# Performance work log

Measured on AMD Instinct MI355X. Metric: run time of the kernel, lower is better.

Reference implementation:

```python
import jax, jax.numpy as jnp
import numpy as np

HEAD_DIM = 64
CLIP = 64  # clipping_distance
B, S = 32, 1024


def setup_inputs() -> dict:
    key = jax.random.key(0)
    kq, kk, kv, km, kt = jax.random.split(key, 5)
    q = jax.random.normal(kq, (B, S, HEAD_DIM), dtype=jnp.float32)
    k = jax.random.normal(kk, (B, S, HEAD_DIM), dtype=jnp.float32)
    v = jax.random.normal(kv, (B, S, HEAD_DIM), dtype=jnp.float32)
    mask = jax.random.randint(km, (B, S, S), 0, 2).astype(jnp.bool_)
    pos_table = jax.random.normal(kt, (2 * CLIP + 1, HEAD_DIM), dtype=jnp.float32)
    return {"q": q, "k": k, "v": v, "mask": mask, "pos_table": pos_table}


def reference(q, k, v, mask, pos_table):
    scaling = 1.0 / np.sqrt(HEAD_DIM).astype(np.float32)
    Sq, Sk = q.shape[1], k.shape[1]
    # relative positions k_idx - q_idx, clipped to [-CLIP, CLIP]
    rel = jnp.arange(Sk)[None, :] - jnp.arange(Sq)[:, None]      # [Sq, Sk]
    idx = jnp.clip(rel, -CLIP, CLIP) + CLIP                      # [Sq, Sk]
    pe = pos_table[idx]                                          # [Sq, Sk, D]
    # content logits + relative positional logits
    logits = jnp.einsum('bqd,bkd->bqk', q, k) + jnp.einsum('bqd,qkd->bqk', q, pe)
    logits = logits * scaling
    logits = jnp.where(mask, -jnp.inf, logits)
    attn = jax.nn.softmax(logits, axis=-1)                       # [B, Sq, Sk]
    return jnp.einsum('bqk,bkd->bqd', attn, v)
```

## Files before the change

kernel.cpp:

```cpp
#include <hip/hip_runtime.h>
#include <stdint.h>

#define BATCH 32
#define SEQ   1024
#define DIM   64
#define NKT   (SEQ / 64)

typedef uint8_t  u8;
typedef uint16_t u16;
typedef uint32_t u32;
typedef unsigned long long u64;
typedef __attribute__((ext_vector_type(8))) __bf16 bf16x8;
typedef __attribute__((ext_vector_type(4))) float  f32x4;
typedef __attribute__((ext_vector_type(4))) u32    u32x4;

__device__ __forceinline__ float fexp2(float x) {
#if __has_builtin(__builtin_amdgcn_exp2f)
    return __builtin_amdgcn_exp2f(x);
#else
    return exp2f(x);
#endif
}

__device__ __forceinline__ u16 f2bf(float f) {
    u32 x = __builtin_bit_cast(u32, f);
    x += 0x7FFFu + ((x >> 16) & 1u);
    return (u16)(x >> 16);
}

__device__ __forceinline__ bf16x8 cvt8(const float* __restrict__ p) {
    f32x4 a = *reinterpret_cast<const f32x4*>(p);
    f32x4 b = *reinterpret_cast<const f32x4*>(p + 4);
    u16 t[8];
    t[0] = f2bf(a[0]); t[1] = f2bf(a[1]); t[2] = f2bf(a[2]); t[3] = f2bf(a[3]);
    t[4] = f2bf(b[0]); t[5] = f2bf(b[1]); t[6] = f2bf(b[2]); t[7] = f2bf(b[3]);
    return __builtin_bit_cast(bf16x8, *reinterpret_cast<u32x4*>(t));
}

__device__ __forceinline__ bf16x8 cvt8s(const float* __restrict__ p, float s) {
    f32x4 a = *reinterpret_cast<const f32x4*>(p);
    f32x4 b = *reinterpret_cast<const f32x4*>(p + 4);
    u16 t[8];
    t[0] = f2bf(a[0] * s); t[1] = f2bf(a[1] * s); t[2] = f2bf(a[2] * s); t[3] = f2bf(a[3] * s);
    t[4] = f2bf(b[0] * s); t[5] = f2bf(b[1] * s); t[6] = f2bf(b[2] * s); t[7] = f2bf(b[3] * s);
    return __builtin_bit_cast(bf16x8, *reinterpret_cast<u32x4*>(t));
}

__device__ __forceinline__ bf16x8 ldg8(const u16* p) {
    u32x4 u = *reinterpret_cast<const u32x4*>(p);
    return __builtin_bit_cast(bf16x8, u);
}

__device__ __forceinline__ u32 pack4(u32x4 a) {
    return (u32)(a[0] != 0) | ((u32)(a[1] != 0) << 8) |
           ((u32)(a[2] != 0) << 16) | ((u32)(a[3] != 0) << 24);
}

__global__ __launch_bounds__(256) void prep_kv(
    const float* __restrict__ kg, const float* __restrict__ vg,
    u16* __restrict__ kb, u16* __restrict__ vtb_) {
    __shared__ u16 tile[64][72];
    const int t  = threadIdx.x;
    const int b  = blockIdx.x >> 4;
    const int k0 = (blockIdx.x & 15) * 64;

    {
        int kk = t >> 2;
        int d0 = (t & 3) * 16;
        const float* src = kg + ((size_t)b * SEQ + k0 + kk) * DIM + d0;
        u16 tmp[16];
#pragma unroll
        for (int i = 0; i < 4; ++i) {
            f32x4 a = *reinterpret_cast<const f32x4*>(src + i * 4);
            tmp[i * 4 + 0] = f2bf(a[0]); tmp[i * 4 + 1] = f2bf(a[1]);
            tmp[i * 4 + 2] = f2bf(a[2]); tmp[i * 4 + 3] = f2bf(a[3]);
        }
        u16* dst = kb + ((size_t)b * SEQ + k0 + kk) * DIM + d0;
        *reinterpret_cast<u32x4*>(dst)     = *reinterpret_cast<u32x4*>(tmp);
        *reinterpret_cast<u32x4*>(dst + 8) = *reinterpret_cast<u32x4*>(tmp + 8);
    }
    {
        const float* vb = vg + (size_t)b * SEQ * DIM;
        int kk = t >> 2;
        int d0 = (t & 3) * 16;
        const float* src = vb + (size_t)(k0 + kk) * DIM + d0;
        u16 tmp[16];
#pragma unroll
        for (int i = 0; i < 4; ++i) {
            f32x4 a = *reinterpret_cast<const f32x4*>(src + i * 4);
            tmp[i * 4 + 0] = f2bf(a[0]); tmp[i * 4 + 1] = f2bf(a[1]);
            tmp[i * 4 + 2] = f2bf(a[2]); tmp[i * 4 + 3] = f2bf(a[3]);
        }
        *reinterpret_cast<u32x4*>(&tile[kk][d0])     = *reinterpret_cast<u32x4*>(tmp);
        *reinterpret_cast<u32x4*>(&tile[kk][d0 + 8]) = *reinterpret_cast<u32x4*>(tmp + 8);
    }
    __syncthreads();
    u16* vtb = vtb_ + (size_t)b * DIM * SEQ;
#pragma unroll
    for (int i = 0; i < 2; ++i) {
        int d  = t / 8 + i * 32;
        int ks = (t % 8) * 8;
        u16 tmp[8];
#pragma unroll
        for (int j = 0; j < 8; ++j) tmp[j] = tile[ks + j][d];
        *reinterpret_cast<u32x4*>(vtb + (size_t)d * SEQ + k0 + ks) =
            *reinterpret_cast<u32x4*>(tmp);
    }
}

__global__ __launch_bounds__(512, 4) void attn_fast8(
    const float* __restrict__ qg, const u16* __restrict__ kbf,
    const u16* __restrict__ vt, const int* __restrict__ maskg,
    const float* __restrict__ ptg, float* __restrict__ outg) {
    __shared__ float qp[64][132];
    __shared__ u16   plds[8][16][72];
    __shared__ u8    mlds[8][16][64];

    const int b    = blockIdx.y;
    const int q0   = blockIdx.x * 64;
    const int tid  = threadIdx.x;
    const int wave = tid >> 6;
    const int lane = tid & 63;
    const int wq   = wave & 3;
    const int wk   = wave >> 2;
    const int quad = lane >> 4;
    const int c16  = lane & 15;

    const float SC = 0.125f * 1.44269504088896340736f;

    const float* qb = qg + ((size_t)b * SEQ + q0) * DIM;

    const bf16x8 qA0 = cvt8s(qb + (size_t)(wq * 16 + c16) * DIM + quad * 8, SC);
    const bf16x8 qA1 = cvt8s(qb + (size_t)(wq * 16 + c16) * DIM + 32 + quad * 8, SC);

    {
        const int jt0 = wk ? 5 : 0, jt1 = wk ? 9 : 5;
        for (int jt = jt0; jt < jt1; ++jt) {
            int j0 = jt * 16;
            int jr = min(j0 + c16, 128);
            bf16x8 b0 = cvt8(ptg + (size_t)jr * DIM + quad * 8);
            bf16x8 b1 = cvt8(ptg + (size_t)jr * DIM + 32 + quad * 8);
            f32x4 acc = {0.f, 0.f, 0.f, 0.f};
            acc = __builtin_amdgcn_mfma_f32_16x16x32_bf16(qA0, b0, acc, 0, 0, 0);
            acc = __builtin_amdgcn_mfma_f32_16x16x32_bf16(qA1, b1, acc, 0, 0, 0);
            int jcol = j0 + c16;
            if (jcol <= 128) {
#pragma unroll
                for (int r = 0; r < 4; ++r)
                    qp[wq * 16 + quad * 4 + r][jcol] = acc[r];
            }
        }
    }
    __syncthreads();

    const u16* kb_base  = kbf + (size_t)b * SEQ * DIM;
    const u16* vtb_base = vt  + (size_t)b * DIM * SEQ;

    const int* mrow = maskg + ((size_t)b * SEQ + q0 + wq * 16 + (lane >> 2)) * SEQ +
                      (lane & 3) * 16;

    u32x4 ma, mbv, mc, md;
    {
        const int* p = mrow + (size_t)(wk * 8) * 64;
        ma  = *reinterpret_cast<const u32x4*>(p);
        mbv = *reinterpret_cast<const u32x4*>(p + 4);
        mc  = *reinterpret_cast<const u32x4*>(p + 8);
        md  = *reinterpret_cast<const u32x4*>(p + 12);
    }

    float l_part[4];
    f32x4 O[4];
#pragma unroll
    for (int r = 0; r < 4; ++r) l_part[r] = 0.f;
#pragma unroll
    for (int d = 0; d < 4; ++d) O[d] = f32x4{0.f, 0.f, 0.f, 0.f};

#pragma unroll
    for (int gg = 0; gg < 2; ++gg) {
#pragma unroll 1
        for (int t = 0; t < 4; ++t) {
            const int kt = wk * 8 + gg * 4 + t;
            const int k0 = kt * 64;

            {
                u32x4 pk;
                pk[0] = pack4(ma); pk[1] = pack4(mbv);
                pk[2] = pack4(mc); pk[3] = pack4(md);
                *reinterpret_cast<u32x4*>(&mlds[wave][lane >> 2][(lane & 3) * 16]) = pk;
            }
            {
                const int* p = mrow + (size_t)((kt + 1) & 15) * 64;
                ma  = *reinterpret_cast<const u32x4*>(p);
                mbv = *reinterpret_cast<const u32x4*>(p + 4);
                mc  = *reinterpret_cast<const u32x4*>(p + 8);
                md  = *reinterpret_cast<const u32x4*>(p + 12);
            }

            f32x4 S[4];
            __builtin_amdgcn_s_setprio(1);
#pragma unroll
            for (int sub = 0; sub < 4; ++sub) {
                const u16* kr = kb_base + (size_t)(k0 + sub * 16 + c16) * DIM;
                bf16x8 kf0 = ldg8(kr + quad * 8);
                bf16x8 kf1 = ldg8(kr + 32 + quad * 8);
                f32x4 acc = {0.f, 0.f, 0.f, 0.f};
                acc = __builtin_amdgcn_mfma_f32_16x16x32_bf16(qA0, kf0, acc, 0, 0, 0);
                acc = __builtin_amdgcn_mfma_f32_16x16x32_bf16(qA1, kf1, acc, 0, 0, 0);
                S[sub] = acc;
            }
            __builtin_amdgcn_s_setprio(0);

#pragma unroll
            for (int r = 0; r < 4; ++r) {
                const int row_l = quad * 4 + r;
                const int row_g = q0 + wq * 16 + row_l;
                float rs = 0.f;
#pragma unroll
                for (int sub = 0; sub < 4; ++sub) {
                    int col_g = k0 + sub * 16 + c16;
                    int rel = col_g - row_g;
                    rel = rel < -64 ? -64 : (rel > 64 ? 64 : rel);
                    float x = S[sub][r] + qp[wq * 16 + row_l][rel + 64];
                    u8 mv = mlds[wave][row_l][sub * 16 + c16];
                    float e = mv ? 0.f : fexp2(x);
                    rs += e;
                    plds[wave][row_l][sub * 16 + c16] = f2bf(e);
                }
                l_part[r] += rs;
            }

            bf16x8 pA0 = *reinterpret_cast<bf16x8*>(&plds[wave][c16][quad * 8]);
            bf16x8 pA1 = *reinterpret_cast<bf16x8*>(&plds[wave][c16][32 + quad * 8]);
            __builtin_amdgcn_s_setprio(1);
#pragma unroll
            for (int d = 0; d < 4; ++d) {
                const u16* vr = vtb_base + (size_t)(d * 16 + c16) * SEQ + k0;
                bf16x8 vf0 = ldg8(vr + quad * 8);
                bf16x8 vf1 = ldg8(vr + 32 + quad * 8);
                O[d] = __builtin_amdgcn_mfma_f32_16x16x32_bf16(pA0, vf0, O[d], 0, 0, 0);
                O[d] = __builtin_amdgcn_mfma_f32_16x16x32_bf16(pA1, vf1, O[d], 0, 0, 0);
            }
            __builtin_amdgcn_s_setprio(0);
        }
    }

    float l_run[4];
#pragma unroll
    for (int r = 0; r < 4; ++r) {
        float rs = l_part[r];
        rs += __shfl_xor(rs, 1);
        rs += __shfl_xor(rs, 2);
        rs += __shfl_xor(rs, 4);
        rs += __shfl_xor(rs, 8);
        l_run[r] = rs;
    }

    __syncthreads();
    float* cmb = &qp[0][0];
    const int cbase = (wq * 64 + lane) * 24;
    if (wk == 1) {
#pragma unroll
        for (int r = 0; r < 4; ++r) cmb[cbase + r] = l_run[r];
#pragma unroll
        for (int d = 0; d < 4; ++d)
#pragma unroll
            for (int r = 0; r < 4; ++r)
                cmb[cbase + 4 + d * 4 + r] = O[d][r];
    }
    __syncthreads();
    if (wk == 0) {
        float* ob = outg + ((size_t)b * SEQ + q0) * DIM;
#pragma unroll
        for (int r = 0; r < 4; ++r) {
            float inv = 1.f / (l_run[r] + cmb[cbase + r]);
            int row_l = wq * 16 + quad * 4 + r;
#pragma unroll
            for (int d = 0; d < 4; ++d) {
                float o = O[d][r] + cmb[cbase + 4 + d * 4 + r];
                ob[(size_t)row_l * DIM + d * 16 + c16] = o * inv;
            }
        }
    }
}

__global__ __launch_bounds__(256) void vt_kernel(const float* __restrict__ v,
                                                 u16* __restrict__ vt) {
    __shared__ u16 tile[64][72];
    const int b  = blockIdx.y;
    const int k0 = blockIdx.x * 64;
    const int t  = threadIdx.x;
    const float* vb  = v  + (size_t)b * SEQ * DIM;
    u16*         vtb = vt + (size_t)b * DIM * SEQ;

    {
        int kk = t >> 2;
        int d0 = (t & 3) * 16;
        const float* src = vb + (size_t)(k0 + kk) * DIM + d0;
        u16 tmp[16];
#pragma unroll
        for (int i = 0; i < 4; ++i) {
            f32x4 a = *reinterpret_cast<const f32x4*>(src + i * 4);
            tmp[i * 4 + 0] = f2bf(a[0]); tmp[i * 4 + 1] = f2bf(a[1]);
            tmp[i * 4 + 2] = f2bf(a[2]); tmp[i * 4 + 3] = f2bf(a[3]);
        }
        *reinterpret_cast<u32x4*>(&tile[kk][d0])     = *reinterpret_cast<u32x4*>(tmp);
        *reinterpret_cast<u32x4*>(&tile[kk][d0 + 8]) = *reinterpret_cast<u32x4*>(tmp + 8);
    }
    __syncthreads();
#pragma unroll
    for (int i = 0; i < 2; ++i) {
        int d  = t / 8 + i * 32;
        int ks = (t % 8) * 8;
        u16 tmp[8];
#pragma unroll
        for (int j = 0; j < 8; ++j) tmp[j] = tile[ks + j][d];
        *reinterpret_cast<u32x4*>(vtb + (size_t)d * SEQ + k0 + ks) =
            *reinterpret_cast<u32x4*>(tmp);
    }
}

template <bool USE_VT>
__global__ __launch_bounds__(256, 2) void attn_kernel(
    const float* __restrict__ qg, const float* __restrict__ kg,
    const void* __restrict__ vgv, const int* __restrict__ maskg,
    const float* __restrict__ ptg, float* __restrict__ outg) {
    __shared__ float qp[64][132];
    __shared__ int   mlds[4][16][68];
    __shared__ u16   plds[4][16][72];

    const int b    = blockIdx.y;
    const int q0   = blockIdx.x * 64;
    const int tid  = threadIdx.x;
    const int wave = tid >> 6;
    const int lane = tid & 63;
    const int quad = lane >> 4;
    const int c16  = lane & 15;

    const float* qb = qg + ((size_t)b * SEQ + q0) * DIM;
    const float* kb = kg + (size_t)b * SEQ * DIM;
    const int*   mb = maskg + ((size_t)b * SEQ + q0) * SEQ;

    const bf16x8 qA0 = cvt8(qb + (size_t)(wave * 16 + c16) * DIM + quad * 8);
    const bf16x8 qA1 = cvt8(qb + (size_t)(wave * 16 + c16) * DIM + 32 + quad * 8);

    for (int jt = 0; jt < 9; ++jt) {
        int j0 = jt * 16;
        int jr = min(j0 + c16, 128);
        bf16x8 b0 = cvt8(ptg + (size_t)jr * DIM + quad * 8);
        bf16x8 b1 = cvt8(ptg + (size_t)jr * DIM + 32 + quad * 8);
        f32x4 acc = {0.f, 0.f, 0.f, 0.f};
        acc = __builtin_amdgcn_mfma_f32_16x16x32_bf16(qA0, b0, acc, 0, 0, 0);
        acc = __builtin_amdgcn_mfma_f32_16x16x32_bf16(qA1, b1, acc, 0, 0, 0);
        int jcol = j0 + c16;
        if (jcol <= 128) {
#pragma unroll
            for (int r = 0; r < 4; ++r)
                qp[wave * 16 + quad * 4 + r][jcol] = acc[r];
        }
    }

    float m_run[4], l_run[4];
    f32x4 O[4];
#pragma unroll
    for (int r = 0; r < 4; ++r) { m_run[r] = -1e30f; l_run[r] = 0.f; }
#pragma unroll
    for (int d = 0; d < 4; ++d) O[d] = f32x4{0.f, 0.f, 0.f, 0.f};

#pragma unroll 1
    for (int kt = 0; kt < NKT; ++kt) {
        const int k0 = kt * 64;
        {
            int row_l = lane >> 2;
            const int* mrow = mb + (size_t)(wave * 16 + row_l) * SEQ + k0;
#pragma unroll
            for (int i = 0; i < 4; ++i) {
                int seg = (lane & 3) + i * 4;
                *reinterpret_cast<u32x4*>(&mlds[wave][row_l][seg * 4]) =
                    *reinterpret_cast<const u32x4*>(mrow + seg * 4);
            }
        }

        f32x4 S[4];
#pragma unroll
        for (int sub = 0; sub < 4; ++sub) {
            const float* kr = kb + (size_t)(k0 + sub * 16 + c16) * DIM;
            bf16x8 kb0 = cvt8(kr + quad * 8);
            bf16x8 kb1 = cvt8(kr + 32 + quad * 8);
            f32x4 acc = {0.f, 0.f, 0.f, 0.f};
            acc = __builtin_amdgcn_mfma_f32_16x16x32_bf16(qA0, kb0, acc, 0, 0, 0);
            acc = __builtin_amdgcn_mfma_f32_16x16x32_bf16(qA1, kb1, acc, 0, 0, 0);
            S[sub] = acc;
        }

        float sv[4][4];
#pragma unroll
        for (int sub = 0; sub < 4; ++sub) {
#pragma unroll
            for (int r = 0; r < 4; ++r) {
                int row_l = quad * 4 + r;
                int row_g = q0 + wave * 16 + row_l;
                int col_g = k0 + sub * 16 + c16;
                int rel = col_g - row_g;
                rel = rel < -64 ? -64 : (rel > 64 ? 64 : rel);
                float x = (S[sub][r] + qp[wave * 16 + row_l][rel + 64]) * 0.125f;
                int mv = mlds[wave][row_l][sub * 16 + c16];
                sv[sub][r] = mv ? -1e30f : x;
            }
        }

        float m_new[4], alpha[4];
#pragma unroll
        for (int r = 0; r < 4; ++r) {
            float rmax = fmaxf(fmaxf(sv[0][r], sv[1][r]), fmaxf(sv[2][r], sv[3][r]));
            rmax = fmaxf(rmax, __shfl_xor(rmax, 1));
            rmax = fmaxf(rmax, __shfl_xor(rmax, 2));
            rmax = fmaxf(rmax, __shfl_xor(rmax, 4));
            rmax = fmaxf(rmax, __shfl_xor(rmax, 8));
            m_new[r] = fmaxf(m_run[r], rmax);
            alpha[r] = __expf(m_run[r] - m_new[r]);
            m_run[r] = m_new[r];
        }
#pragma unroll
        for (int r = 0; r < 4; ++r) {
            float rs = 0.f;
#pragma unroll
            for (int sub = 0; sub < 4; ++sub) {
                float e = __expf(sv[sub][r] - m_new[r]);
                rs += e;
                plds[wave][quad * 4 + r][sub * 16 + c16] = f2bf(e);
            }
            rs += __shfl_xor(rs, 1);
            rs += __shfl_xor(rs, 2);
            rs += __shfl_xor(rs, 4);
            rs += __shfl_xor(rs, 8);
            l_run[r] = l_run[r] * alpha[r] + rs;
#pragma unroll
            for (int d = 0; d < 4; ++d) O[d][r] *= alpha[r];
        }

        bf16x8 pA0 = *reinterpret_cast<bf16x8*>(&plds[wave][c16][quad * 8]);
        bf16x8 pA1 = *reinterpret_cast<bf16x8*>(&plds[wave][c16][32 + quad * 8]);
#pragma unroll
        for (int d = 0; d < 4; ++d) {
            bf16x8 vb0, vb1;
            if (USE_VT) {
                const u16* vtb = (const u16*)vgv + (size_t)b * DIM * SEQ +
                                 (size_t)(d * 16 + c16) * SEQ + k0;
                vb0 = ldg8(vtb + quad * 8);
                vb1 = ldg8(vtb + 32 + quad * 8);
            } else {
                u16 t0[8], t1[8];
                const float* vbase = (const float*)vgv +
                                     ((size_t)b * SEQ + k0) * DIM + d * 16 + c16;
#pragma unroll
                for (int jj = 0; jj < 8; ++jj) {
                    t0[jj] = f2bf(vbase[(size_t)(quad * 8 + jj) * DIM]);
                    t1[jj] = f2bf(vbase[(size_t)(32 + quad * 8 + jj) * DIM]);
                }
                vb0 = __builtin_bit_cast(bf16x8, *reinterpret_cast<u32x4*>(t0));
                vb1 = __builtin_bit_cast(bf16x8, *reinterpret_cast<u32x4*>(t1));
            }
            O[d] = __builtin_amdgcn_mfma_f32_16x16x32_bf16(pA0, vb0, O[d], 0, 0, 0);
            O[d] = __builtin_amdgcn_mfma_f32_16x16x32_bf16(pA1, vb1, O[d], 0, 0, 0);
        }
    }

    float* ob = outg + ((size_t)b * SEQ + q0) * DIM;
#pragma unroll
    for (int r = 0; r < 4; ++r) {
        float inv = 1.f / l_run[r];
        int row_l = wave * 16 + quad * 4 + r;
#pragma unroll
        for (int d = 0; d < 4; ++d)
            ob[(size_t)row_l * DIM + d * 16 + c16] = O[d][r] * inv;
    }
}

extern "C" void kernel_launch(void* const* d_in, const int* in_sizes, int n_in,
                              void* d_out, int out_size, void* d_ws, size_t ws_size,
                              hipStream_t stream) {
    const float* q    = (const float*)d_in[0];
    const float* k    = (const float*)d_in[1];
    const float* v    = (const float*)d_in[2];
    const int*   mask = (const int*)d_in[3];
    const float* pt   = (const float*)d_in[4];
    float* out        = (float*)d_out;

    const size_t vt_bytes = (size_t)BATCH * SEQ * DIM * sizeof(u16);
    const size_t kb_bytes = (size_t)BATCH * SEQ * DIM * sizeof(u16);
    dim3 grid(SEQ / 64, BATCH);

    if (ws_size >= vt_bytes + kb_bytes) {
        u16* vt = (u16*)d_ws;
        u16* kb = (u16*)((char*)d_ws + vt_bytes);
        prep_kv<<<dim3(512), 256, 0, stream>>>(k, v, kb, vt);
        attn_fast8<<<grid, 512, 0, stream>>>(q, kb, vt, mask, pt, out);
    } else if (ws_size >= vt_bytes) {
        u16* vt = (u16*)d_ws;
        vt_kernel<<<grid, 256, 0, stream>>>(v, vt);
        attn_kernel<true><<<grid, 256, 0, stream>>>(q, k, (const void*)vt, mask, pt, out);
    } else {
        attn_kernel<false><<<grid, 256, 0, stream>>>(q, k, (const void*)v, mask, pt, out);
    }
}
```

Baseline: 268.1 us.

## Software-pipeline K/V/mask loads and shortcut clipped positional bias tiles

The attention loop is fully unrolled. K fragments for the next tile are prefetched into registers, the mask is double-buffered two tiles ahead, and V fragments are loaded before the softmax step so memory latency overlaps compute. Tiles far from the diagonal use a per-row constant positional bias (clip at -64 or +64) held in registers, which avoids the per-element relative index and LDS lookup. Launch bounds drop from 4 to 2 blocks per CU to allow the extra registers, which may reduce occupancy.

```diff
diff --git a/kernel.cpp b/kernel.cpp
--- a/kernel.cpp
+++ b/kernel.cpp
@@ -108,7 +108,7 @@
     }
 }
 
-__global__ __launch_bounds__(512, 4) void attn_fast8(
+__global__ __launch_bounds__(512, 2) void attn_fast9(
     const float* __restrict__ qg, const u16* __restrict__ kbf,
     const u16* __restrict__ vt, const int* __restrict__ maskg,
     const float* __restrict__ ptg, float* __restrict__ outg) {
@@ -153,19 +153,37 @@
     }
     __syncthreads();
 
+    float cL[4], cR[4];
+#pragma unroll
+    for (int r = 0; r < 4; ++r) {
+        cL[r] = qp[wq * 16 + quad * 4 + r][0];
+        cR[r] = qp[wq * 16 + quad * 4 + r][128];
+    }
+
     const u16* kb_base  = kbf + (size_t)b * SEQ * DIM;
     const u16* vtb_base = vt  + (size_t)b * DIM * SEQ;
+    const int  row_min  = q0 + wq * 16;
+    const int  ktbase   = wk * 8;
 
     const int* mrow = maskg + ((size_t)b * SEQ + q0 + wq * 16 + (lane >> 2)) * SEQ +
                       (lane & 3) * 16;
 
-    u32x4 ma, mbv, mc, md;
-    {
-        const int* p = mrow + (size_t)(wk * 8) * 64;
-        ma  = *reinterpret_cast<const u32x4*>(p);
-        mbv = *reinterpret_cast<const u32x4*>(p + 4);
-        mc  = *reinterpret_cast<const u32x4*>(p + 8);
-        md  = *reinterpret_cast<const u32x4*>(p + 12);
+    u32x4 mreg[2][4];
+#pragma unroll
+    for (int s = 0; s < 2; ++s) {
+        const int* p = mrow + (size_t)(ktbase + s) * 64;
+        mreg[s][0] = *reinterpret_cast<const u32x4*>(p);
+        mreg[s][1] = *reinterpret_cast<const u32x4*>(p + 4);
+        mreg[s][2] = *reinterpret_cast<const u32x4*>(p + 8);
+        mreg[s][3] = *reinterpret_cast<const u32x4*>(p + 12);
+    }
+
+    bf16x8 kc0[4], kc1[4];
+#pragma unroll
+    for (int sub = 0; sub < 4; ++sub) {
+        const u16* kr = kb_base + (size_t)(ktbase * 64 + sub * 16 + c16) * DIM;
+        kc0[sub] = ldg8(kr + quad * 8);
+        kc1[sub] = ldg8(kr + 32 + quad * 8);
     }
 
     float l_part[4];
@@ -176,44 +194,77 @@
     for (int d = 0; d < 4; ++d) O[d] = f32x4{0.f, 0.f, 0.f, 0.f};
 
 #pragma unroll
-    for (int gg = 0; gg < 2; ++gg) {
-#pragma unroll 1
-        for (int t = 0; t < 4; ++t) {
-            const int kt = wk * 8 + gg * 4 + t;
-            const int k0 = kt * 64;
-
-            {
-                u32x4 pk;
-                pk[0] = pack4(ma); pk[1] = pack4(mbv);
-                pk[2] = pack4(mc); pk[3] = pack4(md);
-                *reinterpret_cast<u32x4*>(&mlds[wave][lane >> 2][(lane & 3) * 16]) = pk;
-            }
-            {
-                const int* p = mrow + (size_t)((kt + 1) & 15) * 64;
-                ma  = *reinterpret_cast<const u32x4*>(p);
-                mbv = *reinterpret_cast<const u32x4*>(p + 4);
-                mc  = *reinterpret_cast<const u32x4*>(p + 8);
-                md  = *reinterpret_cast<const u32x4*>(p + 12);
-            }
-
-            f32x4 S[4];
-            __builtin_amdgcn_s_setprio(1);
+    for (int j = 0; j < 8; ++j) {
+        const int kt = ktbase + j;
+        const int k0 = kt * 64;
+        const int ms = j & 1;
+
+        {
+            u32x4 pk;
+            pk[0] = pack4(mreg[ms][0]); pk[1] = pack4(mreg[ms][1]);
+            pk[2] = pack4(mreg[ms][2]); pk[3] = pack4(mreg[ms][3]);
+            *reinterpret_cast<u32x4*>(&mlds[wave][lane >> 2][(lane & 3) * 16]) = pk;
+        }
+        {
+            const int* p = mrow + (size_t)((kt + 2) & 15) * 64;
+            mreg[ms][0] = *reinterpret_cast<const u32x4*>(p);
+            mreg[ms][1] = *reinterpret_cast<const u32x4*>(p + 4);
+            mreg[ms][2] = *reinterpret_cast<const u32x4*>(p + 8);
+            mreg[ms][3] = *reinterpret_cast<const u32x4*>(p + 12);
+        }
+
+        f32x4 S[4];
+        __builtin_amdgcn_s_setprio(1);
+#pragma unroll
+        for (int sub = 0; sub < 4; ++sub) {
+            f32x4 acc = {0.f, 0.f, 0.f, 0.f};
+            acc = __builtin_amdgcn_mfma_f32_16x16x32_bf16(qA0, kc0[sub], acc, 0, 0, 0);
+            acc = __builtin_amdgcn_mfma_f32_16x16x32_bf16(qA1, kc1[sub], acc, 0, 0, 0);
+            S[sub] = acc;
+        }
+        __builtin_amdgcn_s_setprio(0);
+
+        {
+            const int kn = (ktbase + ((j + 1) & 7)) * 64;
 #pragma unroll
             for (int sub = 0; sub < 4; ++sub) {
-                const u16* kr = kb_base + (size_t)(k0 + sub * 16 + c16) * DIM;
-                bf16x8 kf0 = ldg8(kr + quad * 8);
-                bf16x8 kf1 = ldg8(kr + 32 + quad * 8);
-                f32x4 acc = {0.f, 0.f, 0.f, 0.f};
-                acc = __builtin_amdgcn_mfma_f32_16x16x32_bf16(qA0, kf0, acc, 0, 0, 0);
-                acc = __builtin_amdgcn_mfma_f32_16x16x32_bf16(qA1, kf1, acc, 0, 0, 0);
-                S[sub] = acc;
-            }
-            __builtin_amdgcn_s_setprio(0);
-
+                const u16* kr = kb_base + (size_t)(kn + sub * 16 + c16) * DIM;
+                kc0[sub] = ldg8(kr + quad * 8);
+                kc1[sub] = ldg8(kr + 32 + quad * 8);
+            }
+        }
+
+        bf16x8 vf0[4], vf1[4];
+#pragma unroll
+        for (int d = 0; d < 4; ++d) {
+            const u16* vr = vtb_base + (size_t)(d * 16 + c16) * SEQ + k0;
+            vf0[d] = ldg8(vr + quad * 8);
+            vf1[d] = ldg8(vr + 32 + quad * 8);
+        }
+
+        const bool farL = (k0 + 127 <= row_min);
+        const bool farR = (k0 >= row_min + 79);
+
+        if (farL | farR) {
 #pragma unroll
             for (int r = 0; r < 4; ++r) {
                 const int row_l = quad * 4 + r;
-                const int row_g = q0 + wq * 16 + row_l;
+                const float c = farL ? cL[r] : cR[r];
+                float rs = 0.f;
+#pragma unroll
+                for (int sub = 0; sub < 4; ++sub) {
+                    u8 mv = mlds[wave][row_l][sub * 16 + c16];
+                    float e = mv ? 0.f : fexp2(S[sub][r] + c);
+                    rs += e;
+                    plds[wave][row_l][sub * 16 + c16] = f2bf(e);
+                }
+                l_part[r] += rs;
+            }
+        } else {
+#pragma unroll
+            for (int r = 0; r < 4; ++r) {
+                const int row_l = quad * 4 + r;
+                const int row_g = row_min + row_l;
                 float rs = 0.f;
 #pragma unroll
                 for (int sub = 0; sub < 4; ++sub) {
@@ -228,20 +279,17 @@
                 }
                 l_part[r] += rs;
             }
-
-            bf16x8 pA0 = *reinterpret_cast<bf16x8*>(&plds[wave][c16][quad * 8]);
-            bf16x8 pA1 = *reinterpret_cast<bf16x8*>(&plds[wave][c16][32 + quad * 8]);
-            __builtin_amdgcn_s_setprio(1);
-#pragma unroll
-            for (int d = 0; d < 4; ++d) {
-                const u16* vr = vtb_base + (size_t)(d * 16 + c16) * SEQ + k0;
-                bf16x8 vf0 = ldg8(vr + quad * 8);
-                bf16x8 vf1 = ldg8(vr + 32 + quad * 8);
-                O[d] = __builtin_amdgcn_mfma_f32_16x16x32_bf16(pA0, vf0, O[d], 0, 0, 0);
-                O[d] = __builtin_amdgcn_mfma_f32_16x16x32_bf16(pA1, vf1, O[d], 0, 0, 0);
-            }
-            __builtin_amdgcn_s_setprio(0);
-        }
+        }
+
+        bf16x8 pA0 = *reinterpret_cast<bf16x8*>(&plds[wave][c16][quad * 8]);
+        bf16x8 pA1 = *reinterpret_cast<bf16x8*>(&plds[wave][c16][32 + quad * 8]);
+        __builtin_amdgcn_s_setprio(1);
+#pragma unroll
+        for (int d = 0; d < 4; ++d) {
+            O[d] = __builtin_amdgcn_mfma_f32_16x16x32_bf16(pA0, vf0[d], O[d], 0, 0, 0);
+            O[d] = __builtin_amdgcn_mfma_f32_16x16x32_bf16(pA1, vf1[d], O[d], 0, 0, 0);
+        }
+        __builtin_amdgcn_s_setprio(0);
     }
 
     float l_run[4];
@@ -494,7 +542,7 @@
         u16* vt = (u16*)d_ws;
         u16* kb = (u16*)((char*)d_ws + vt_bytes);
         prep_kv<<<dim3(512), 256, 0, stream>>>(k, v, kb, vt);
-        attn_fast8<<<grid, 512, 0, stream>>>(q, kb, vt, mask, pt, out);
+        attn_fast9<<<grid, 512, 0, stream>>>(q, kb, vt, mask, pt, out);
     } else if (ws_size >= vt_bytes) {
         u16* vt = (u16*)d_ws;
         vt_kernel<<<grid, 256, 0, stream>>>(v, vt);
```

After: 258.3 us. -3.7%, faster.
